# Kernel optimization log

Hardware: AMD Instinct MI355X
Metric: run time of the kernel (lower is better)

## Reference

```python
import jax, jax.numpy as jnp
import numpy as np

D_MODEL = 1024
N_HEADS = 16
HEAD_DIM = D_MODEL // N_HEADS
BATCH = 2
SEQ = 2048
MASK_FILL = -10000.0


def setup_inputs() -> dict:
    key = jax.random.key(0)
    ks = jax.random.split(key, 5)
    scale = 1.0 / np.sqrt(D_MODEL)
    return {
        "x": jax.random.normal(ks[0], (BATCH, SEQ, D_MODEL), dtype=jnp.float32),
        "w_q": jax.random.normal(ks[1], (D_MODEL, D_MODEL), dtype=jnp.float32) * scale,
        "w_k": jax.random.normal(ks[2], (D_MODEL, D_MODEL), dtype=jnp.float32) * scale,
        "w_v": jax.random.normal(ks[3], (D_MODEL, D_MODEL), dtype=jnp.float32) * scale,
        "w_o": jax.random.normal(ks[4], (D_MODEL, D_MODEL), dtype=jnp.float32) * scale,
    }


def reference(x, w_q, w_k, w_v, w_o):
    B, S, C = x.shape
    # Linear(bias=False): y = x @ W^T (torch stores W as [out, in])
    q = jnp.einsum("bsc,dc->bsd", x, w_q).reshape(B, S, N_HEADS, HEAD_DIM)
    k = jnp.einsum("bsc,dc->bsd", x, w_k).reshape(B, S, N_HEADS, HEAD_DIM)
    v = jnp.einsum("bsc,dc->bsd", x, w_v).reshape(B, S, N_HEADS, HEAD_DIM)
    # scores: [B, H, S, S]
    scores = jnp.einsum("bqhd,bkhd->bhqk", q, k) / np.sqrt(HEAD_DIM)
    causal = jnp.tril(jnp.ones((S, S), dtype=bool))
    scores = jnp.where(causal, scores, MASK_FILL)
    weights = jax.nn.softmax(scores, axis=-1)
    out = jnp.einsum("bhqk,bkhd->bqhd", weights, v).reshape(B, S, C)
    return jnp.einsum("bsc,dc->bsd", out, w_o)
```

## Files before the change

### kernel.cpp

```cpp
#include <hip/hip_runtime.h>

typedef __attribute__((ext_vector_type(8))) short bf16x8;
typedef __attribute__((ext_vector_type(4))) float floatx4;

static constexpr int SEQ    = 2048;
static constexpr int CDIM   = 1024;
static constexpr int NH     = 16;
static constexpr int HD     = 64;
static constexpr int NBATCH = 2;
static constexpr int MROWS  = NBATCH * SEQ;

static __device__ __forceinline__ short f2bf(float f) {
    union { float f; unsigned u; } x; x.f = f;
    unsigned r = x.u + 0x7fffu + ((x.u >> 16) & 1u);
    return (short)(r >> 16);
}

static __device__ __forceinline__ unsigned pack2bf(float lo, float hi) {
    return ((unsigned)(unsigned short)f2bf(hi) << 16) | (unsigned)(unsigned short)f2bf(lo);
}

static __device__ __forceinline__ unsigned pk2(float lo, float hi) {
    union { float f; unsigned u; } a, b; a.f = lo; b.f = hi;
    return __builtin_amdgcn_perm(b.u + 0x8000u, a.u + 0x8000u, 0x07060302u);
}

static __device__ __forceinline__ float bf2f(short s) {
    union { unsigned u; float f; } x;
    x.u = ((unsigned)(unsigned short)s) << 16;
    return x.f;
}

static __device__ __forceinline__ floatx4 mfma16(bf16x8 a, bf16x8 b, floatx4 c) {
    return __builtin_amdgcn_mfma_f32_16x16x32_bf16(a, b, c, 0, 0, 0);
}

static __device__ __forceinline__ bf16x8 mk8(unsigned d0, unsigned d1, unsigned d2, unsigned d3) {
    union { unsigned u[4]; bf16x8 v; } x;
    x.u[0] = d0; x.u[1] = d1; x.u[2] = d2; x.u[3] = d3;
    return x.v;
}

static __device__ __forceinline__ void gl_lds16(const short* g, short* l) {
    __builtin_amdgcn_global_load_lds(
        (const __attribute__((address_space(1))) void*)g,
        (__attribute__((address_space(3))) void*)l, 16, 0, 0);
}

__global__ void convert_all(
    const void* __restrict__ x,  const void* __restrict__ wq,
    const void* __restrict__ wk, const void* __restrict__ wv,
    const void* __restrict__ wo,
    short* __restrict__ xc,  short* __restrict__ wqc, short* __restrict__ wkc,
    short* __restrict__ wvc, short* __restrict__ woc,
    int* __restrict__ flag)
{
    const int tid = threadIdx.x;
    const unsigned short* xs = (const unsigned short*)x;
    int pl = 0;
    for (int i = tid; i < 2048; i += 256) {
        const int e = (xs[2 * i] >> 7) & 0xFF;
        if (e >= 110 && e <= 144) pl++;
    }
    #pragma unroll
    for (int off = 32; off > 0; off >>= 1) pl += __shfl_down(pl, off, 64);
    __shared__ int cnt;
    if (tid == 0) cnt = 0;
    __syncthreads();
    if ((tid & 63) == 0) atomicAdd(&cnt, pl);
    __syncthreads();
    const int f = (cnt < 1024) ? 1 : 0;
    if (blockIdx.x == 0 && blockIdx.y == 0 && tid == 0) *flag = f;

    const int y = blockIdx.y;
    const void* src = (y == 0) ? x  : (y == 1) ? wq : (y == 2) ? wk : (y == 3) ? wv : wo;
    short*      dst = (y == 0) ? xc : (y == 1) ? wqc : (y == 2) ? wkc : (y == 3) ? wvc : woc;
    const int n4 = (y == 0) ? (MROWS * CDIM / 4) : (CDIM * CDIM / 4);

    const int stride = gridDim.x * blockDim.x;
    for (int i = blockIdx.x * blockDim.x + tid; i < n4; i += stride) {
        if (f) {
            const float4 v = ((const float4*)src)[i];
            ((uint2*)dst)[i] = make_uint2(pack2bf(v.x, v.y), pack2bf(v.z, v.w));
        } else {
            ((uint2*)dst)[i] = ((const uint2*)src)[i];
        }
    }
}

__global__ __launch_bounds__(256) void gemm_bt128(
    const short* __restrict__ A,
    const short* __restrict__ W0, const short* __restrict__ W1, const short* __restrict__ W2,
    void* __restrict__ C0, void* __restrict__ C1, void* __restrict__ C2,
    short* __restrict__ VT, const int* __restrict__ flag)
{
    const int m0  = blockIdx.x * 128;
    const int sel = blockIdx.y >> 3;
    const int n0  = (blockIdx.y & 7) * 128;
    const short* W = (sel == 0) ? W0 : ((sel == 1) ? W1 : W2);
    void*        C = (sel == 0) ? C0 : ((sel == 1) ? C1 : C2);
    const bool f32out = (flag != nullptr) && (*flag != 0);
    const bool vtout  = (sel == 2) && (VT != nullptr);

    __shared__ __align__(16) short ta[128 * 64];
    __shared__ __align__(16) short tb[128 * 64];

    const int tid  = threadIdx.x;
    const int lane = tid & 63;
    const int wave = tid >> 6;
    const int quad = lane >> 4;
    const int l16  = lane & 15;
    const int wm   = (wave >> 1) * 64;
    const int wn   = (wave & 1) * 64;

    floatx4 acc[4][4];
    #pragma unroll
    for (int i = 0; i < 4; i++)
        #pragma unroll
        for (int j = 0; j < 4; j++)
            acc[i][j] = 0.0f;

    const int sr8 = lane >> 3;
    const int ug  = ((lane & 7) ^ sr8) * 8;
    const short* Ab = A + (size_t)(m0 + 32 * wave + sr8) * CDIM + ug;
    const short* Wb = W + (size_t)(n0 + 32 * wave + sr8) * CDIM + ug;
    short* ta0 = ta + (32 * wave) * 64;
    short* tb0 = tb + (32 * wave) * 64;

    for (int k0 = 0; k0 < CDIM; k0 += 64) {
        __syncthreads();
        gl_lds16(Ab + k0,             ta0);
        gl_lds16(Ab +  8 * CDIM + k0, ta0 +  8 * 64);
        gl_lds16(Ab + 16 * CDIM + k0, ta0 + 16 * 64);
        gl_lds16(Ab + 24 * CDIM + k0, ta0 + 24 * 64);
        gl_lds16(Wb + k0,             tb0);
        gl_lds16(Wb +  8 * CDIM + k0, tb0 +  8 * 64);
        gl_lds16(Wb + 16 * CDIM + k0, tb0 + 16 * 64);
        gl_lds16(Wb + 24 * CDIM + k0, tb0 + 24 * 64);
        __syncthreads();

        #pragma unroll
        for (int kc = 0; kc < 2; kc++) {
            const int pu = (((kc * 4 + quad) ^ (l16 & 7))) * 8;
            bf16x8 af[4], bw[4];
            #pragma unroll
            for (int i = 0; i < 4; i++)
                af[i] = *(const bf16x8*)(ta + (wm + i * 16 + l16) * 64 + pu);
            #pragma unroll
            for (int j = 0; j < 4; j++)
                bw[j] = *(const bf16x8*)(tb + (wn + j * 16 + l16) * 64 + pu);
            #pragma unroll
            for (int i = 0; i < 4; i++)
                #pragma unroll
                for (int j = 0; j < 4; j++)
                    acc[i][j] = mfma16(af[i], bw[j], acc[i][j]);
        }
    }

    #pragma unroll
    for (int i = 0; i < 4; i++) {
        #pragma unroll
        for (int j = 0; j < 4; j++) {
            const int row0 = m0 + wm + i * 16 + quad * 4;
            const int col  = n0 + wn + j * 16 + l16;
            if (vtout) {
                const int bb  = row0 >> 11;
                const int key = row0 & 2047;
                const size_t idx = ((size_t)(bb * 1024 + col)) * 2048 + key;
                *(uint2*)(VT + idx) = make_uint2(pk2(acc[i][j][0], acc[i][j][1]),
                                                 pk2(acc[i][j][2], acc[i][j][3]));
            } else if (f32out) {
                float* cp = (float*)C + (size_t)row0 * CDIM + col;
                #pragma unroll
                for (int r = 0; r < 4; r++)
                    cp[(size_t)r * CDIM] = acc[i][j][r];
            } else {
                short* cp = (short*)C + (size_t)row0 * CDIM + col;
                #pragma unroll
                for (int r = 0; r < 4; r++)
                    cp[(size_t)r * CDIM] = f2bf(acc[i][j][r]);
            }
        }
    }
}

__global__ __launch_bounds__(256) void gemm_n64(
    const short* __restrict__ A, const short* __restrict__ W,
    void* __restrict__ C, const int* __restrict__ flag)
{
    const int m0 = blockIdx.x * 128;
    const int n0 = blockIdx.y * 64;
    const bool f32out = (flag != nullptr) && (*flag != 0);

    __shared__ __align__(16) short ta[128 * 64];
    __shared__ __align__(16) short tb[64 * 64];

    const int tid  = threadIdx.x;
    const int lane = tid & 63;
    const int wave = tid >> 6;
    const int quad = lane >> 4;
    const int l16  = lane & 15;
    const int wm   = (wave >> 1) * 64;
    const int wn   = (wave & 1) * 32;

    floatx4 acc[4][2];
    #pragma unroll
    for (int i = 0; i < 4; i++)
        #pragma unroll
        for (int j = 0; j < 2; j++)
            acc[i][j] = 0.0f;

    const int sr8 = lane >> 3;
    const int ug  = ((lane & 7) ^ sr8) * 8;
    const short* Ab = A + (size_t)(m0 + 32 * wave + sr8) * CDIM + ug;
    const short* Wb = W + (size_t)(n0 + 16 * wave + sr8) * CDIM + ug;
    short* ta0 = ta + (32 * wave) * 64;
    short* tb0 = tb + (16 * wave) * 64;

    for (int k0 = 0; k0 < CDIM; k0 += 64) {
        __syncthreads();
        gl_lds16(Ab + k0,             ta0);
        gl_lds16(Ab +  8 * CDIM + k0, ta0 +  8 * 64);
        gl_lds16(Ab + 16 * CDIM + k0, ta0 + 16 * 64);
        gl_lds16(Ab + 24 * CDIM + k0, ta0 + 24 * 64);
        gl_lds16(Wb + k0,             tb0);
        gl_lds16(Wb +  8 * CDIM + k0, tb0 +  8 * 64);
        __syncthreads();

        #pragma unroll
        for (int kc = 0; kc < 2; kc++) {
            const int pu = (((kc * 4 + quad) ^ (l16 & 7))) * 8;
            bf16x8 af[4], bw[2];
            #pragma unroll
            for (int i = 0; i < 4; i++)
                af[i] = *(const bf16x8*)(ta + (wm + i * 16 + l16) * 64 + pu);
            #pragma unroll
            for (int j = 0; j < 2; j++)
                bw[j] = *(const bf16x8*)(tb + (wn + j * 16 + l16) * 64 + pu);
            #pragma unroll
            for (int i = 0; i < 4; i++)
                #pragma unroll
                for (int j = 0; j < 2; j++)
                    acc[i][j] = mfma16(af[i], bw[j], acc[i][j]);
        }
    }

    #pragma unroll
    for (int i = 0; i < 4; i++) {
        #pragma unroll
        for (int j = 0; j < 2; j++) {
            const int row0 = m0 + wm + i * 16 + quad * 4;
            const int col  = n0 + wn + j * 16 + l16;
            if (f32out) {
                float* cp = (float*)C + (size_t)row0 * CDIM + col;
                #pragma unroll
                for (int r = 0; r < 4; r++)
                    cp[(size_t)r * CDIM] = acc[i][j][r];
            } else {
                short* cp = (short*)C + (size_t)row0 * CDIM + col;
                #pragma unroll
                for (int r = 0; r < 4; r++)
                    cp[(size_t)r * CDIM] = f2bf(acc[i][j][r]);
            }
        }
    }
}

__global__ __launch_bounds__(256, 2) void attn_t(
    const short* __restrict__ Q, const short* __restrict__ K,
    const short* __restrict__ VT,
    short* __restrict__ P0, short* __restrict__ P1, float* __restrict__ L)
{
    const int h = blockIdx.x;
    const int b = blockIdx.y;
    const int z = blockIdx.z;
    const int g = z >> 3;
    const int item = (g == 1) ? (23 - z) : (g == 3) ? (55 - z) : z;
    const int qt2 = 15 - (item >> 1);
    const int p   = item & 1;
    const int nktall = qt2 + 1;

    const int tid  = threadIdx.x;
    const int lane = tid & 63;
    const int wave = tid >> 6;
    const int quad = lane >> 4;
    const int l16  = lane & 15;

    __shared__ __align__(16) short Kt[128][72];
    __shared__ __align__(16) short Vt[64][136];

    const int rowBase = b * SEQ;
    const int colH    = h * HD;
    const int qgA     = qt2 * 128 + wave * 16 + l16;
    const int qgB     = qgA + 64;

    bf16x8 qa0, qa1, qc0, qc1;
    {
        const short* qp = Q + (size_t)(rowBase + qgA) * CDIM + colH + quad * 8;
        qa0 = *(const bf16x8*)qp;
        qa1 = *(const bf16x8*)(qp + 32);
        const short* qp2 = qp + (size_t)64 * CDIM;
        qc0 = *(const bf16x8*)qp2;
        qc1 = *(const bf16x8*)(qp2 + 32);
    }

    floatx4 oA[4], oB[4];
    #pragma unroll
    for (int nd = 0; nd < 4; nd++) { oA[nd] = 0.0f; oB[nd] = 0.0f; }
    floatx4 lAv = 0.0f, lBv = 0.0f;
    const bf16x8 ones = mk8(0x3F803F80u, 0x3F803F80u, 0x3F803F80u, 0x3F803F80u);

    const int kk = tid >> 1;
    const int kd = (tid & 1) * 32;
    const short* kg = K + (size_t)(rowBase + kk) * CDIM + colH + kd;
    const int sd = tid >> 2;
    const int sk = (tid & 3) * 32;
    const short* vg = VT + ((size_t)(b * NH + h) * HD + sd) * SEQ + sk;

    const short* kg0 = kg + (size_t)p * 128 * CDIM;
    const short* vg0 = vg + p * 128;
    uint4 ka_0 = *(const uint4*)(kg0);
    uint4 ka_1 = *(const uint4*)(kg0 + 8);
    uint4 ka_2 = *(const uint4*)(kg0 + 16);
    uint4 ka_3 = *(const uint4*)(kg0 + 24);
    uint4 va_0 = *(const uint4*)(vg0);
    uint4 va_1 = *(const uint4*)(vg0 + 8);
    uint4 va_2 = *(const uint4*)(vg0 + 16);
    uint4 va_3 = *(const uint4*)(vg0 + 24);

    const float SCL = 0.18033688011112042f;

    for (int kt = p; kt < nktall; kt += 2) {
        __syncthreads();
        *(uint4*)&Kt[kk][kd]      = ka_0;
        *(uint4*)&Kt[kk][kd + 8]  = ka_1;
        *(uint4*)&Kt[kk][kd + 16] = ka_2;
        *(uint4*)&Kt[kk][kd + 24] = ka_3;
        {
            short* vrow = &Vt[sd][sk];
            *(uint2*)(vrow + 0)  = make_uint2(va_0.x, va_0.y);
            *(uint2*)(vrow + 8)  = make_uint2(va_0.z, va_0.w);
            *(uint2*)(vrow + 16) = make_uint2(va_1.x, va_1.y);
            *(uint2*)(vrow + 24) = make_uint2(va_1.z, va_1.w);
            *(uint2*)(vrow + 4)  = make_uint2(va_2.x, va_2.y);
            *(uint2*)(vrow + 12) = make_uint2(va_2.z, va_2.w);
            *(uint2*)(vrow + 20) = make_uint2(va_3.x, va_3.y);
            *(uint2*)(vrow + 28) = make_uint2(va_3.z, va_3.w);
        }
        __syncthreads();

        if (kt + 2 < nktall) {
            const short* kn = kg + (size_t)(kt + 2) * 128 * CDIM;
            const short* vn = vg + (kt + 2) * 128;
            ka_0 = *(const uint4*)(kn);
            ka_1 = *(const uint4*)(kn + 8);
            ka_2 = *(const uint4*)(kn + 16);
            ka_3 = *(const uint4*)(kn + 24);
            va_0 = *(const uint4*)(vn);
            va_1 = *(const uint4*)(vn + 8);
            va_2 = *(const uint4*)(vn + 16);
            va_3 = *(const uint4*)(vn + 24);
        }

        const int key0 = kt * 128;
        const bool masked = (kt == nktall - 1);

        unsigned hA0 = 0, hA1 = 0, hB0 = 0, hB1 = 0;
        #pragma unroll
        for (int ms = 0; ms < 8; ms++) {
            const short* kp = &Kt[ms * 16 + l16][quad * 8];
            bf16x8 k0 = *(const bf16x8*)kp;
            bf16x8 k1 = *(const bf16x8*)(kp + 32);
            floatx4 sA = {0.f, 0.f, 0.f, 0.f};
            floatx4 sB = {0.f, 0.f, 0.f, 0.f};
            __builtin_amdgcn_s_setprio(1);
            sA = mfma16(k0, qa0, sA);
            sB = mfma16(k0, qc0, sB);
            sA = mfma16(k1, qa1, sA);
            sB = mfma16(k1, qc1, sB);
            __builtin_amdgcn_s_setprio(0);
            float pA[4], pB[4];
            #pragma unroll
            for (int r = 0; r < 4; r++) {
                const int kgl = key0 + ms * 16 + quad * 4 + r;
                float eA = __builtin_amdgcn_exp2f(sA[r] * SCL);
                float eB = __builtin_amdgcn_exp2f(sB[r] * SCL);
                if (masked) {
                    if (kgl > qgA) eA = 0.0f;
                    if (kgl > qgB) eB = 0.0f;
                }
                pA[r] = eA;
                pB[r] = eB;
            }
            const unsigned cA0 = pk2(pA[0], pA[1]);
            const unsigned cA1 = pk2(pA[2], pA[3]);
            const unsigned cB0 = pk2(pB[0], pB[1]);
            const unsigned cB1 = pk2(pB[2], pB[3]);
            if ((ms & 1) == 0) {
                hA0 = cA0; hA1 = cA1; hB0 = cB0; hB1 = cB1;
            } else {
                const int kc = ms >> 1;
                const bf16x8 pbA = mk8(hA0, hA1, cA0, cA1);
                const bf16x8 pbB = mk8(hB0, hB1, cB0, cB1);
                __builtin_amdgcn_s_setprio(1);
                #pragma unroll
                for (int nd = 0; nd < 4; nd++) {
                    const bf16x8 va = *(const bf16x8*)&Vt[nd * 16 + l16][kc * 32 + quad * 8];
                    oA[nd] = mfma16(va, pbA, oA[nd]);
                    oB[nd] = mfma16(va, pbB, oB[nd]);
                }
                lAv = mfma16(ones, pbA, lAv);
                lBv = mfma16(ones, pbB, lBv);
                __builtin_amdgcn_s_setprio(0);
            }
        }
    }

    const float lA = lAv[0];
    const float lB = lBv[0];

    short* Pp = p ? P1 : P0;
    float* Lp = L + p * (NBATCH * NH * SEQ);
    short* opA = Pp + (size_t)(rowBase + qgA) * CDIM + colH;
    short* opB = Pp + (size_t)(rowBase + qgB) * CDIM + colH;
    #pragma unroll
    for (int nd = 0; nd < 4; nd++) {
        *(uint2*)(opA + nd * 16 + quad * 4) =
            make_uint2(pk2(oA[nd][0], oA[nd][1]), pk2(oA[nd][2], oA[nd][3]));
        *(uint2*)(opB + nd * 16 + quad * 4) =
            make_uint2(pk2(oB[nd][0], oB[nd][1]), pk2(oB[nd][2], oB[nd][3]));
    }
    if (quad == 0) {
        Lp[(b * NH + h) * SEQ + qgA] = lA;
        Lp[(b * NH + h) * SEQ + qgB] = lB;
    }
}

__global__ void combine(const short* __restrict__ P0, const short* __restrict__ P1,
                        const float* __restrict__ L, short* __restrict__ Ob)
{
    const int i = blockIdx.x * blockDim.x + threadIdx.x;
    const int row = i >> 7;
    const int c8  = i & 127;
    const int h   = c8 >> 3;
    const int b   = row >> 11;
    const int q   = row & 2047;
    const int li  = (b * NH + h) * SEQ + q;
    const float inv = 1.0f / (L[li] + L[NBATCH * NH * SEQ + li]);

    const bf16x8 a0 = ((const bf16x8*)P0)[i];
    const bf16x8 a1 = ((const bf16x8*)P1)[i];
    unsigned d[4];
    #pragma unroll
    for (int e = 0; e < 4; e++) {
        const float lo = (bf2f(a0[2 * e])     + bf2f(a1[2 * e]))     * inv;
        const float hi = (bf2f(a0[2 * e + 1]) + bf2f(a1[2 * e + 1])) * inv;
        d[e] = pk2(lo, hi);
    }
    ((uint4*)Ob)[i] = make_uint4(d[0], d[1], d[2], d[3]);
}

extern "C" void kernel_launch(void* const* d_in, const int* in_sizes, int n_in,
                              void* d_out, int out_size, void* d_ws, size_t ws_size,
                              hipStream_t stream)
{
    const void* x  = d_in[0];
    const void* wq = d_in[1];
    const void* wk = d_in[2];
    const void* wv = d_in[3];
    const void* wo = d_in[4];

    int* flag = (int*)d_ws;
    short* w = (short*)((char*)d_ws + 256);
    const int ME  = 1024 * 1024;
    short* Wqc = w;
    short* Wkc = w + 1 * ME;
    short* Wvc = w + 2 * ME;
    short* Woc = w + 3 * ME;
    short* Xc  = w + 4 * ME;
    short* Qb  = w + 8 * ME;
    short* Kb  = w + 12 * ME;
    short* VTb = w + 16 * ME;
    short* P1b = w + 20 * ME;
    float* Lb  = (float*)(w + 24 * ME);
    short* P0b = Xc;
    short* Ob  = Xc;

    dim3 blk(256);
    convert_all<<<dim3(512, 5), blk, 0, stream>>>(
        x, wq, wk, wv, wo, Xc, Wqc, Wkc, Wvc, Woc, flag);

    gemm_bt128<<<dim3(MROWS / 128, 24), blk, 0, stream>>>(
        Xc, Wqc, Wkc, Wvc, Qb, Kb, nullptr, VTb, nullptr);
    attn_t<<<dim3(NH, NBATCH, 32), blk, 0, stream>>>(Qb, Kb, VTb, P0b, P1b, Lb);
    combine<<<dim3(MROWS * CDIM / 8 / 256), blk, 0, stream>>>(P0b, P1b, Lb, Ob);
    gemm_n64<<<dim3(MROWS / 128, CDIM / 64), blk, 0, stream>>>(
        Ob, Woc, d_out, flag);
}
```

Measured before the change: 168.5 us.

## Remap GEMM tiles per XCD for L2 locality and fold softmax scale into Q

```diff
diff --git a/kernel.cpp b/kernel.cpp
--- a/kernel.cpp
+++ b/kernel.cpp
@@ -94,13 +94,19 @@
     void* __restrict__ C0, void* __restrict__ C1, void* __restrict__ C2,
     short* __restrict__ VT, const int* __restrict__ flag)
 {
-    const int m0  = blockIdx.x * 128;
-    const int sel = blockIdx.y >> 3;
-    const int n0  = (blockIdx.y & 7) * 128;
+    const int lid = blockIdx.y * gridDim.x + blockIdx.x;
+    const int xcd = lid & 7;
+    const int r   = lid >> 3;
+    const int mt  = ((xcd >> 2) << 4) + (r & 15);
+    const int yt  = (xcd & 3) * 6 + (r >> 4);
+    const int m0  = mt * 128;
+    const int sel = yt >> 3;
+    const int n0  = (yt & 7) * 128;
     const short* W = (sel == 0) ? W0 : ((sel == 1) ? W1 : W2);
     void*        C = (sel == 0) ? C0 : ((sel == 1) ? C1 : C2);
     const bool f32out = (flag != nullptr) && (*flag != 0);
     const bool vtout  = (sel == 2) && (VT != nullptr);
+    const float oscl  = (sel == 0) ? 0.18033688011112042f : 1.0f;
 
     __shared__ __align__(16) short ta[128 * 64];
     __shared__ __align__(16) short tb[128 * 64];
@@ -172,13 +178,13 @@
             } else if (f32out) {
                 float* cp = (float*)C + (size_t)row0 * CDIM + col;
                 #pragma unroll
-                for (int r = 0; r < 4; r++)
-                    cp[(size_t)r * CDIM] = acc[i][j][r];
+                for (int r2 = 0; r2 < 4; r2++)
+                    cp[(size_t)r2 * CDIM] = acc[i][j][r2];
             } else {
                 short* cp = (short*)C + (size_t)row0 * CDIM + col;
                 #pragma unroll
-                for (int r = 0; r < 4; r++)
-                    cp[(size_t)r * CDIM] = f2bf(acc[i][j][r]);
+                for (int r2 = 0; r2 < 4; r2++)
+                    cp[(size_t)r2 * CDIM] = f2bf(acc[i][j][r2] * oscl);
             }
         }
     }
@@ -188,8 +194,13 @@
     const short* __restrict__ A, const short* __restrict__ W,
     void* __restrict__ C, const int* __restrict__ flag)
 {
-    const int m0 = blockIdx.x * 128;
-    const int n0 = blockIdx.y * 64;
+    const int lid = blockIdx.y * gridDim.x + blockIdx.x;
+    const int xcd = lid & 7;
+    const int r   = lid >> 3;
+    const int mt  = ((xcd >> 1) << 3) + (r & 7);
+    const int nt  = ((xcd & 1) << 3) + (r >> 3);
+    const int m0  = mt * 128;
+    const int n0  = nt * 64;
     const bool f32out = (flag != nullptr) && (*flag != 0);
 
     __shared__ __align__(16) short ta[128 * 64];
@@ -254,13 +265,13 @@
             if (f32out) {
                 float* cp = (float*)C + (size_t)row0 * CDIM + col;
                 #pragma unroll
-                for (int r = 0; r < 4; r++)
-                    cp[(size_t)r * CDIM] = acc[i][j][r];
+                for (int r2 = 0; r2 < 4; r2++)
+                    cp[(size_t)r2 * CDIM] = acc[i][j][r2];
             } else {
                 short* cp = (short*)C + (size_t)row0 * CDIM + col;
                 #pragma unroll
-                for (int r = 0; r < 4; r++)
-                    cp[(size_t)r * CDIM] = f2bf(acc[i][j][r]);
+                for (int r2 = 0; r2 < 4; r2++)
+                    cp[(size_t)r2 * CDIM] = f2bf(acc[i][j][r2]);
             }
         }
     }
@@ -327,8 +338,6 @@
     uint4 va_1 = *(const uint4*)(vg0 + 8);
     uint4 va_2 = *(const uint4*)(vg0 + 16);
     uint4 va_3 = *(const uint4*)(vg0 + 24);
-
-    const float SCL = 0.18033688011112042f;
 
     for (int kt = p; kt < nktall; kt += 2) {
         __syncthreads();
@@ -383,8 +392,8 @@
             #pragma unroll
             for (int r = 0; r < 4; r++) {
                 const int kgl = key0 + ms * 16 + quad * 4 + r;
-                float eA = __builtin_amdgcn_exp2f(sA[r] * SCL);
-                float eB = __builtin_amdgcn_exp2f(sB[r] * SCL);
+                float eA = __builtin_amdgcn_exp2f(sA[r]);
+                float eB = __builtin_amdgcn_exp2f(sB[r]);
                 if (masked) {
                     if (kgl > qgA) eA = 0.0f;
                     if (kgl > qgB) eB = 0.0f;
```

Result: slower. 181.6 us (+7.8%).
